# Kernel tuning notes

Hardware: AMD Instinct MI355X
Metric: run time of the kernel (lower is better)

## Reference

```python
import jax, jax.numpy as jnp
import numpy as np

NUM_EMBEDDINGS = 1024
EMBEDDING_DIM = 256
COMMITMENT_COST = 0.25
DECAY = 0.99
EPS = 1e-05
BATCH = 65536


def setup_inputs() -> dict:
    key = jax.random.key(0)
    k1, k2 = jax.random.split(key, 2)
    z_e = jax.random.normal(k1, (BATCH, EMBEDDING_DIM), dtype=jnp.float32)
    embedding = jax.random.normal(k2, (NUM_EMBEDDINGS, EMBEDDING_DIM), dtype=jnp.float32)
    ema_cluster_size = jnp.zeros((NUM_EMBEDDINGS,), dtype=jnp.float32)
    ema_w = embedding  # buffer initialized as a clone of the codebook
    return {"z_e": z_e, "embedding": embedding,
            "ema_cluster_size": ema_cluster_size, "ema_w": ema_w}


def reference(z_e, embedding, ema_cluster_size, ema_w):
    B, D = z_e.shape
    K = embedding.shape[0]

    # Squared L2 distances: ||z||^2 + ||e||^2 - 2 z.e  -> [B, K]
    z_sq = jnp.sum(z_e * z_e, axis=1, keepdims=True)          # [B, 1]
    e_sq = jnp.sum(embedding * embedding, axis=1)[None, :]    # [1, K]
    ze = jnp.matmul(z_e, embedding.T)                         # [B, K]
    distances = z_sq + e_sq - 2.0 * ze

    encoding_indices = jnp.argmin(distances, axis=1)          # [B]

    # Gather instead of one-hot matmul (same math as encodings @ embedding)
    z_q = embedding[encoding_indices]                         # [B, D]
    z_q_st = z_e + jax.lax.stop_gradient(z_q - z_e)

    vq_loss = COMMITMENT_COST * jnp.mean(
        (jax.lax.stop_gradient(z_q) - z_e) ** 2)

    # EMA statistics (training-mode update); segment_sum == one-hot reductions
    cluster_size = jax.ops.segment_sum(
        jnp.ones((B,), dtype=z_e.dtype), encoding_indices, num_segments=K)
    new_ema_cluster_size = DECAY * ema_cluster_size + (1.0 - DECAY) * cluster_size
    dw = jax.ops.segment_sum(z_e, encoding_indices, num_segments=K)  # [K, D]
    new_ema_w = DECAY * ema_w + (1.0 - DECAY) * dw

    n = jnp.sum(new_ema_cluster_size)
    smoothed = (new_ema_cluster_size + EPS) / (n + K * EPS) * n
    new_embedding = new_ema_w / smoothed[:, None]

    avg_probs = cluster_size / B
    perplexity = jnp.exp(-jnp.sum(avg_probs * jnp.log(avg_probs + 1e-10)))

    return (z_q_st, vq_loss, perplexity, encoding_indices,
            new_embedding, new_ema_cluster_size, new_ema_w)
```

## Files before the change

### kernel.cpp

```cpp
#include <hip/hip_runtime.h>
#include <hip/hip_bf16.h>
#include <math.h>

#define BATCH 65536
#define DIM 256
#define KC 1024
#define COMMIT 0.25f
#define DECAY 0.99f
#define EPSV 1e-5f

#define O_ZQ   0
#define O_LOSS 16777216
#define O_PERP 16777217
#define O_IDX  16777218
#define O_EMB  16842754
#define O_NCS  17104898
#define O_NEW  17105922

typedef __attribute__((ext_vector_type(8))) short bf16x8;
typedef __attribute__((ext_vector_type(4))) float f32x4;

typedef __attribute__((address_space(1))) const void* as1_cvp;
typedef __attribute__((address_space(3))) void* as3_vp;

__device__ __forceinline__ void gload_lds16(const void* g, void* l) {
    __builtin_amdgcn_global_load_lds((as1_cvp)g, (as3_vp)l, 16, 0, 0);
}

__device__ __forceinline__ unsigned short bf16_rne(float x) {
    unsigned u = __builtin_bit_cast(unsigned, x);
    unsigned r = (u + 0x7FFFu + ((u >> 16) & 1u)) >> 16;
    return (unsigned short)r;
}
__device__ __forceinline__ float bf16_to_f(unsigned short h) {
    unsigned u = ((unsigned)h) << 16;
    return __builtin_bit_cast(float, u);
}

__global__ __launch_bounds__(256) void zero_kernel(float* __restrict__ dw,
                                                   int* __restrict__ counts,
                                                   float* __restrict__ loss_part) {
    int i = blockIdx.x * 256 + threadIdx.x;
    if (i < KC * DIM) dw[i] = 0.0f;
    if (i < KC) counts[i] = 0;
    if (i < 256) loss_part[i] = 0.0f;
}

__global__ __launch_bounds__(64) void prep_kernel(const float* __restrict__ emb,
                                                  unsigned short* __restrict__ ehi,
                                                  unsigned short* __restrict__ elo,
                                                  float* __restrict__ e_sq) {
    int k = blockIdx.x;
    int lane = threadIdx.x;
    const float4* ep = (const float4*)(emb + (size_t)k * DIM);
    float4 e = ep[lane];
    float x[4] = {e.x, e.y, e.z, e.w};
    unsigned h[4], l[4];
    float s = 0.0f;
    #pragma unroll
    for (int j = 0; j < 4; ++j) {
        h[j] = bf16_rne(x[j]);
        l[j] = bf16_rne(x[j] - bf16_to_f((unsigned short)h[j]));
        s += x[j] * x[j];
    }
    uint2 ph = make_uint2(h[0] | (h[1] << 16), h[2] | (h[3] << 16));
    uint2 pl = make_uint2(l[0] | (l[1] << 16), l[2] | (l[3] << 16));
    int slot = lane >> 1;
    int half = lane & 1;
    int us = k * 256 + ((slot ^ (k & 7)) << 3) + (half << 2);
    *(uint2*)(ehi + us) = ph;
    *(uint2*)(elo + us) = pl;
    for (int off = 32; off; off >>= 1) s += __shfl_down(s, off, 64);
    if (lane == 0) e_sq[k] = s;
}

#define CH_ROWS 64
__global__ __launch_bounds__(256, 2) void argmin_kernel(
        const float* __restrict__ z_e,
        const unsigned short* __restrict__ ehi,
        const unsigned short* __restrict__ elo,
        const float* __restrict__ e_sq,
        int* __restrict__ idx_out, float* __restrict__ idx_f_out,
        int* __restrict__ counts) {
    __shared__ __align__(16) unsigned short bhi_s[CH_ROWS * 256];
    __shared__ __align__(16) unsigned short blo_s[CH_ROWS * 256];
    __shared__ float esq_s[KC];

    int tid = threadIdx.x;
    int w = tid >> 6;
    int lane = tid & 63;
    int m16 = lane & 15;
    int quad = lane >> 4;
    int base_m = blockIdx.x * 128 + w * 32;

    #pragma unroll
    for (int i = 0; i < 4; ++i) esq_s[tid + i * 256] = e_sq[tid + i * 256];

    bf16x8 ahi[2][8], alo[2][8];
    #pragma unroll
    for (int f = 0; f < 2; ++f) {
        const float* zr = z_e + (size_t)(base_m + f * 16 + m16) * DIM;
        #pragma unroll
        for (int ks = 0; ks < 8; ++ks) {
            const float4* p = (const float4*)(zr + ks * 32 + quad * 8);
            float4 x0 = p[0], x1 = p[1];
            float xs[8] = {x0.x, x0.y, x0.z, x0.w, x1.x, x1.y, x1.z, x1.w};
            #pragma unroll
            for (int j = 0; j < 8; ++j) {
                unsigned short h = bf16_rne(xs[j]);
                unsigned short l = bf16_rne(xs[j] - bf16_to_f(h));
                ahi[f][ks][j] = (short)h;
                alo[f][ks][j] = (short)l;
            }
        }
    }

    float best0[4] = {1e30f, 1e30f, 1e30f, 1e30f};
    float best1[4] = {1e30f, 1e30f, 1e30f, 1e30f};
    int bk0[4] = {0, 0, 0, 0};
    int bk1[4] = {0, 0, 0, 0};

    const int rsw = (m16 & 7) << 3;

    for (int chunk = 0; chunk < 16; ++chunk) {
        __syncthreads();
        {
            const char* gh = (const char*)ehi + chunk * 32768 + tid * 16;
            const char* gl = (const char*)elo + chunk * 32768 + tid * 16;
            char* lh = (char*)bhi_s + tid * 16;
            char* ll = (char*)blo_s + tid * 16;
            #pragma unroll
            for (int r = 0; r < 8; ++r) {
                gload_lds16(gh + r * 4096, lh + r * 4096);
                gload_lds16(gl + r * 4096, ll + r * 4096);
            }
        }
        __syncthreads();

        #pragma unroll
        for (int f = 0; f < 4; ++f) {
            f32x4 acc0 = {0.f, 0.f, 0.f, 0.f};
            f32x4 acc1 = {0.f, 0.f, 0.f, 0.f};
            const unsigned short* bh_row = bhi_s + (f * 16 + m16) * 256;
            const unsigned short* bl_row = blo_s + (f * 16 + m16) * 256;
            #pragma unroll
            for (int ks = 0; ks < 8; ++ks) {
                int us_off = (((ks * 4 + quad) << 3) ^ rsw);
                bf16x8 bh = *(const bf16x8*)(bh_row + us_off);
                bf16x8 bl = *(const bf16x8*)(bl_row + us_off);
                acc0 = __builtin_amdgcn_mfma_f32_16x16x32_bf16(ahi[0][ks], bh, acc0, 0, 0, 0);
                acc1 = __builtin_amdgcn_mfma_f32_16x16x32_bf16(ahi[1][ks], bh, acc1, 0, 0, 0);
                acc0 = __builtin_amdgcn_mfma_f32_16x16x32_bf16(ahi[0][ks], bl, acc0, 0, 0, 0);
                acc1 = __builtin_amdgcn_mfma_f32_16x16x32_bf16(ahi[1][ks], bl, acc1, 0, 0, 0);
                acc0 = __builtin_amdgcn_mfma_f32_16x16x32_bf16(alo[0][ks], bh, acc0, 0, 0, 0);
                acc1 = __builtin_amdgcn_mfma_f32_16x16x32_bf16(alo[1][ks], bh, acc1, 0, 0, 0);
            }
            int col = chunk * 64 + f * 16 + m16;
            float es = esq_s[col];
            #pragma unroll
            for (int r = 0; r < 4; ++r) {
                float d0 = es - 2.0f * acc0[r];
                float d1 = es - 2.0f * acc1[r];
                if (d0 < best0[r]) { best0[r] = d0; bk0[r] = col; }
                if (d1 < best1[r]) { best1[r] = d1; bk1[r] = col; }
            }
        }
    }

    #pragma unroll
    for (int off = 1; off < 16; off <<= 1) {
        #pragma unroll
        for (int r = 0; r < 4; ++r) {
            float ov0 = __shfl_xor(best0[r], off, 64);
            int   ok0 = __shfl_xor(bk0[r], off, 64);
            if (ov0 < best0[r] || (ov0 == best0[r] && ok0 < bk0[r])) { best0[r] = ov0; bk0[r] = ok0; }
            float ov1 = __shfl_xor(best1[r], off, 64);
            int   ok1 = __shfl_xor(bk1[r], off, 64);
            if (ov1 < best1[r] || (ov1 == best1[r] && ok1 < bk1[r])) { best1[r] = ov1; bk1[r] = ok1; }
        }
    }
    if (m16 == 0) {
        #pragma unroll
        for (int r = 0; r < 4; ++r) {
            int row0 = base_m + quad * 4 + r;
            int row1 = base_m + 16 + quad * 4 + r;
            idx_out[row0] = bk0[r];
            idx_f_out[row0] = (float)bk0[r];
            idx_out[row1] = bk1[r];
            idx_f_out[row1] = (float)bk1[r];
            atomicAdd(&counts[bk0[r]], 1);
            atomicAdd(&counts[bk1[r]], 1);
        }
    }
}

__global__ __launch_bounds__(1024) void prefix_kernel(const int* __restrict__ counts,
                                                      int* __restrict__ cursor) {
    __shared__ int sc[KC];
    int t = threadIdx.x;
    int c = counts[t];
    sc[t] = c;
    __syncthreads();
    for (int off = 1; off < KC; off <<= 1) {
        int v = 0;
        if (t >= off) v = sc[t - off];
        __syncthreads();
        if (t >= off) sc[t] += v;
        __syncthreads();
    }
    cursor[t] = sc[t] - c;
}

__global__ __launch_bounds__(256) void scatter_rows_kernel(
        const int* __restrict__ idx, int* __restrict__ cursor,
        int* __restrict__ sorted_rows) {
    int i = blockIdx.x * 256 + threadIdx.x;
    int k = idx[i];
    int pos = atomicAdd(&cursor[k], 1);
    sorted_rows[pos] = i;
}

#define SEG 64
__global__ __launch_bounds__(256) void dw_zq_kernel(
        const float* __restrict__ z_e, const float* __restrict__ emb,
        const int* __restrict__ idx, const int* __restrict__ sorted_rows,
        float* __restrict__ zq_out, float* __restrict__ dw,
        float* __restrict__ loss_part) {
    __shared__ int rows_s[SEG];
    __shared__ int keys_s[SEG];
    int t = threadIdx.x;
    int base = blockIdx.x * SEG;
    if (t < SEG) {
        int r = sorted_rows[base + t];
        rows_s[t] = r;
        keys_s[t] = idx[r];
    }
    __syncthreads();

    float acc = 0.0f;
    float lsum = 0.0f;
    int kprev = keys_s[0];
    for (int g = 0; g < SEG / 8; ++g) {
        int rowb[8], kb[8];
        float zb[8], qb[8];
        #pragma unroll
        for (int u = 0; u < 8; ++u) {
            int i = g * 8 + u;
            rowb[u] = rows_s[i];
            kb[u] = keys_s[i];
        }
        #pragma unroll
        for (int u = 0; u < 8; ++u) {
            zb[u] = z_e[(size_t)rowb[u] * DIM + t];
            qb[u] = emb[(size_t)kb[u] * DIM + t];
        }
        #pragma unroll
        for (int u = 0; u < 8; ++u) {
            float z = zb[u];
            float d = qb[u] - z;
            zq_out[(size_t)rowb[u] * DIM + t] = z + d;
            lsum += d * d;
            int k = kb[u];
            if (k != kprev) {
                atomicAdd(&dw[(size_t)kprev * DIM + t], acc);
                acc = 0.0f;
                kprev = k;
            }
            acc += z;
        }
    }
    atomicAdd(&dw[(size_t)kprev * DIM + t], acc);

    __shared__ float red[256];
    red[t] = lsum;
    __syncthreads();
    for (int s = 128; s; s >>= 1) {
        if (t < s) red[t] += red[t + s];
        __syncthreads();
    }
    if (t == 0) atomicAdd(&loss_part[blockIdx.x & 255], red[0]);
}

__global__ __launch_bounds__(1024) void finalize_cluster(
        const float* __restrict__ ema_cs, const int* __restrict__ counts,
        const float* __restrict__ loss_part, float* __restrict__ out,
        float* __restrict__ n_ws) {
    __shared__ float s1[1024];
    __shared__ float s2[1024];
    __shared__ float s3[1024];
    int t = threadIdx.x;
    float c = (float)counts[t];
    float ncs = DECAY * ema_cs[t] + (1.0f - DECAY) * c;
    out[O_NCS + t] = ncs;
    float p = c / (float)BATCH;
    s1[t] = ncs;
    s2[t] = p * logf(p + 1e-10f);
    s3[t] = (t < 256) ? loss_part[t] : 0.0f;
    __syncthreads();
    for (int s = 512; s; s >>= 1) {
        if (t < s) { s1[t] += s1[t + s]; s2[t] += s2[t + s]; s3[t] += s3[t + s]; }
        __syncthreads();
    }
    if (t == 0) {
        n_ws[0] = s1[0];
        out[O_PERP] = expf(-s2[0]);
        out[O_LOSS] = COMMIT * s3[0] / (float)((size_t)BATCH * DIM);
    }
}

__global__ __launch_bounds__(256) void finalize_emb(
        const float* __restrict__ ema_w, const float* __restrict__ dw,
        const float* __restrict__ ncs_arr, const float* __restrict__ n_ws,
        float* __restrict__ out_emb, float* __restrict__ out_emaw) {
    int k = blockIdx.x;
    int d = threadIdx.x;
    size_t i = (size_t)k * DIM + d;
    float w = DECAY * ema_w[i] + (1.0f - DECAY) * dw[i];
    out_emaw[i] = w;
    float n = n_ws[0];
    float ncs = ncs_arr[k];
    float smoothed = (ncs + EPSV) / (n + (float)KC * EPSV) * n;
    out_emb[i] = w / smoothed;
}

extern "C" void kernel_launch(void* const* d_in, const int* in_sizes, int n_in,
                              void* d_out, int out_size, void* d_ws, size_t ws_size,
                              hipStream_t stream) {
    const float* z_e    = (const float*)d_in[0];
    const float* emb    = (const float*)d_in[1];
    const float* ema_cs = (const float*)d_in[2];
    const float* ema_w  = (const float*)d_in[3];
    float* out = (float*)d_out;
    float* ws = (float*)d_ws;

    float* dw            = ws;
    unsigned short* ehi  = (unsigned short*)(dw + KC * DIM);
    unsigned short* elo  = ehi + KC * DIM;
    float* e_sq          = (float*)(elo + KC * DIM);
    int* idx             = (int*)(e_sq + KC);
    int* counts          = idx + BATCH;
    int* cursor          = counts + KC;
    int* sorted_rows     = cursor + KC;
    float* loss_part     = (float*)(sorted_rows + BATCH);
    float* n_ws          = loss_part + 256;

    zero_kernel<<<dim3(1024), dim3(256), 0, stream>>>(dw, counts, loss_part);
    prep_kernel<<<dim3(KC), dim3(64), 0, stream>>>(emb, ehi, elo, e_sq);
    argmin_kernel<<<dim3(BATCH / 128), dim3(256), 0, stream>>>(
        z_e, ehi, elo, e_sq, idx, out + O_IDX, counts);
    prefix_kernel<<<dim3(1), dim3(1024), 0, stream>>>(counts, cursor);
    scatter_rows_kernel<<<dim3(BATCH / 256), dim3(256), 0, stream>>>(
        idx, cursor, sorted_rows);
    dw_zq_kernel<<<dim3(BATCH / SEG), dim3(256), 0, stream>>>(
        z_e, emb, idx, sorted_rows, out + O_ZQ, dw, loss_part);
    finalize_cluster<<<dim3(1), dim3(1024), 0, stream>>>(
        ema_cs, counts, loss_part, out, n_ws);
    finalize_emb<<<dim3(KC), dim3(256), 0, stream>>>(
        ema_w, dw, out + O_NCS, n_ws, out + O_EMB, out + O_NEW);
}
```

Before: 300.1 us.

## Double-buffer codebook chunks in argmin, fuse prep/zero, vectorize dw and scan

The argmin kernel now splits the codebook into 32-row chunks held in two LDS buffers, so the next chunk's global-to-LDS load is issued while the current chunk runs on MFMA. The zero and prep kernels are merged into one launch. The prefix scan uses wave shuffles instead of a barrier-heavy shared-memory loop. The gather/scatter kernel has each wave handle 16 sorted rows with float4 loads, which cuts per-thread load count but issues four scalar atomics per flush.

```diff
diff --git a/kernel.cpp b/kernel.cpp
--- a/kernel.cpp
+++ b/kernel.cpp
@@ -37,44 +37,42 @@
     return __builtin_bit_cast(float, u);
 }
 
-__global__ __launch_bounds__(256) void zero_kernel(float* __restrict__ dw,
-                                                   int* __restrict__ counts,
-                                                   float* __restrict__ loss_part) {
-    int i = blockIdx.x * 256 + threadIdx.x;
-    if (i < KC * DIM) dw[i] = 0.0f;
-    if (i < KC) counts[i] = 0;
-    if (i < 256) loss_part[i] = 0.0f;
-}
-
-__global__ __launch_bounds__(64) void prep_kernel(const float* __restrict__ emb,
-                                                  unsigned short* __restrict__ ehi,
-                                                  unsigned short* __restrict__ elo,
-                                                  float* __restrict__ e_sq) {
+__global__ __launch_bounds__(256) void prep_zero_kernel(
+        const float* __restrict__ emb,
+        unsigned short* __restrict__ ehi, unsigned short* __restrict__ elo,
+        float* __restrict__ e_sq, float* __restrict__ dw,
+        int* __restrict__ counts, float* __restrict__ loss_part) {
     int k = blockIdx.x;
-    int lane = threadIdx.x;
-    const float4* ep = (const float4*)(emb + (size_t)k * DIM);
-    float4 e = ep[lane];
-    float x[4] = {e.x, e.y, e.z, e.w};
-    unsigned h[4], l[4];
-    float s = 0.0f;
-    #pragma unroll
-    for (int j = 0; j < 4; ++j) {
-        h[j] = bf16_rne(x[j]);
-        l[j] = bf16_rne(x[j] - bf16_to_f((unsigned short)h[j]));
-        s += x[j] * x[j];
-    }
-    uint2 ph = make_uint2(h[0] | (h[1] << 16), h[2] | (h[3] << 16));
-    uint2 pl = make_uint2(l[0] | (l[1] << 16), l[2] | (l[3] << 16));
-    int slot = lane >> 1;
-    int half = lane & 1;
-    int us = k * 256 + ((slot ^ (k & 7)) << 3) + (half << 2);
-    *(uint2*)(ehi + us) = ph;
-    *(uint2*)(elo + us) = pl;
-    for (int off = 32; off; off >>= 1) s += __shfl_down(s, off, 64);
-    if (lane == 0) e_sq[k] = s;
-}
-
-#define CH_ROWS 64
+    int t = threadIdx.x;
+    dw[(size_t)k * DIM + t] = 0.0f;
+    if (t == 64) counts[k] = 0;
+    if (k < 2 && t >= 128) loss_part[k * 128 + (t - 128)] = 0.0f;
+    if (t < 64) {
+        int lane = t;
+        const float4* ep = (const float4*)(emb + (size_t)k * DIM);
+        float4 e = ep[lane];
+        float x[4] = {e.x, e.y, e.z, e.w};
+        unsigned h[4], l[4];
+        float s = 0.0f;
+        #pragma unroll
+        for (int j = 0; j < 4; ++j) {
+            h[j] = bf16_rne(x[j]);
+            l[j] = bf16_rne(x[j] - bf16_to_f((unsigned short)h[j]));
+            s += x[j] * x[j];
+        }
+        uint2 ph = make_uint2(h[0] | (h[1] << 16), h[2] | (h[3] << 16));
+        uint2 pl = make_uint2(l[0] | (l[1] << 16), l[2] | (l[3] << 16));
+        int slot = lane >> 1;
+        int half = lane & 1;
+        int us = k * 256 + ((slot ^ (k & 7)) << 3) + (half << 2);
+        *(uint2*)(ehi + us) = ph;
+        *(uint2*)(elo + us) = pl;
+        for (int off = 32; off; off >>= 1) s += __shfl_down(s, off, 64);
+        if (lane == 0) e_sq[k] = s;
+    }
+}
+
+#define CH_ROWS 32
 __global__ __launch_bounds__(256, 2) void argmin_kernel(
         const float* __restrict__ z_e,
         const unsigned short* __restrict__ ehi,
@@ -82,8 +80,8 @@
         const float* __restrict__ e_sq,
         int* __restrict__ idx_out, float* __restrict__ idx_f_out,
         int* __restrict__ counts) {
-    __shared__ __align__(16) unsigned short bhi_s[CH_ROWS * 256];
-    __shared__ __align__(16) unsigned short blo_s[CH_ROWS * 256];
+    __shared__ __align__(16) unsigned short bhi_s[2][CH_ROWS * 256];
+    __shared__ __align__(16) unsigned short blo_s[2][CH_ROWS * 256];
     __shared__ float esq_s[KC];
 
     int tid = threadIdx.x;
@@ -92,6 +90,17 @@
     int m16 = lane & 15;
     int quad = lane >> 4;
     int base_m = blockIdx.x * 128 + w * 32;
+
+#define STAGE(c, b) { \
+    const char* gh_ = (const char*)ehi + (c) * 16384 + tid * 16; \
+    const char* gl_ = (const char*)elo + (c) * 16384 + tid * 16; \
+    char* lh_ = (char*)(bhi_s[b]) + tid * 16; \
+    char* ll_ = (char*)(blo_s[b]) + tid * 16; \
+    _Pragma("unroll") for (int r_ = 0; r_ < 4; ++r_) { \
+        gload_lds16(gh_ + r_ * 4096, lh_ + r_ * 4096); \
+        gload_lds16(gl_ + r_ * 4096, ll_ + r_ * 4096); } }
+
+    STAGE(0, 0)
 
     #pragma unroll
     for (int i = 0; i < 4; ++i) esq_s[tid + i * 256] = e_sq[tid + i * 256];
@@ -122,49 +131,39 @@
 
     const int rsw = (m16 & 7) << 3;
 
-    for (int chunk = 0; chunk < 16; ++chunk) {
+#define COMPUTE(c, b) { \
+    _Pragma("unroll") for (int f_ = 0; f_ < 2; ++f_) { \
+        f32x4 acc0 = {0.f, 0.f, 0.f, 0.f}; \
+        f32x4 acc1 = {0.f, 0.f, 0.f, 0.f}; \
+        const unsigned short* bh_row = bhi_s[b] + (f_ * 16 + m16) * 256; \
+        const unsigned short* bl_row = blo_s[b] + (f_ * 16 + m16) * 256; \
+        _Pragma("unroll") for (int ks_ = 0; ks_ < 8; ++ks_) { \
+            int us_off = (((ks_ * 4 + quad) << 3) ^ rsw); \
+            bf16x8 bh = *(const bf16x8*)(bh_row + us_off); \
+            bf16x8 bl = *(const bf16x8*)(bl_row + us_off); \
+            acc0 = __builtin_amdgcn_mfma_f32_16x16x32_bf16(ahi[0][ks_], bh, acc0, 0, 0, 0); \
+            acc1 = __builtin_amdgcn_mfma_f32_16x16x32_bf16(ahi[1][ks_], bh, acc1, 0, 0, 0); \
+            acc0 = __builtin_amdgcn_mfma_f32_16x16x32_bf16(ahi[0][ks_], bl, acc0, 0, 0, 0); \
+            acc1 = __builtin_amdgcn_mfma_f32_16x16x32_bf16(ahi[1][ks_], bl, acc1, 0, 0, 0); \
+            acc0 = __builtin_amdgcn_mfma_f32_16x16x32_bf16(alo[0][ks_], bh, acc0, 0, 0, 0); \
+            acc1 = __builtin_amdgcn_mfma_f32_16x16x32_bf16(alo[1][ks_], bh, acc1, 0, 0, 0); } \
+        int col = (c) * 32 + f_ * 16 + m16; \
+        float es = esq_s[col]; \
+        _Pragma("unroll") for (int r_ = 0; r_ < 4; ++r_) { \
+            float d0 = es - 2.0f * acc0[r_]; \
+            float d1 = es - 2.0f * acc1[r_]; \
+            if (d0 < best0[r_]) { best0[r_] = d0; bk0[r_] = col; } \
+            if (d1 < best1[r_]) { best1[r_] = d1; bk1[r_] = col; } } } }
+
+    __syncthreads();
+
+    for (int c = 0; c < 32; c += 2) {
+        STAGE(c + 1, 1)
+        COMPUTE(c, 0)
         __syncthreads();
-        {
-            const char* gh = (const char*)ehi + chunk * 32768 + tid * 16;
-            const char* gl = (const char*)elo + chunk * 32768 + tid * 16;
-            char* lh = (char*)bhi_s + tid * 16;
-            char* ll = (char*)blo_s + tid * 16;
-            #pragma unroll
-            for (int r = 0; r < 8; ++r) {
-                gload_lds16(gh + r * 4096, lh + r * 4096);
-                gload_lds16(gl + r * 4096, ll + r * 4096);
-            }
-        }
+        if (c + 2 < 32) STAGE(c + 2, 0)
+        COMPUTE(c + 1, 1)
         __syncthreads();
-
-        #pragma unroll
-        for (int f = 0; f < 4; ++f) {
-            f32x4 acc0 = {0.f, 0.f, 0.f, 0.f};
-            f32x4 acc1 = {0.f, 0.f, 0.f, 0.f};
-            const unsigned short* bh_row = bhi_s + (f * 16 + m16) * 256;
-            const unsigned short* bl_row = blo_s + (f * 16 + m16) * 256;
-            #pragma unroll
-            for (int ks = 0; ks < 8; ++ks) {
-                int us_off = (((ks * 4 + quad) << 3) ^ rsw);
-                bf16x8 bh = *(const bf16x8*)(bh_row + us_off);
-                bf16x8 bl = *(const bf16x8*)(bl_row + us_off);
-                acc0 = __builtin_amdgcn_mfma_f32_16x16x32_bf16(ahi[0][ks], bh, acc0, 0, 0, 0);
-                acc1 = __builtin_amdgcn_mfma_f32_16x16x32_bf16(ahi[1][ks], bh, acc1, 0, 0, 0);
-                acc0 = __builtin_amdgcn_mfma_f32_16x16x32_bf16(ahi[0][ks], bl, acc0, 0, 0, 0);
-                acc1 = __builtin_amdgcn_mfma_f32_16x16x32_bf16(ahi[1][ks], bl, acc1, 0, 0, 0);
-                acc0 = __builtin_amdgcn_mfma_f32_16x16x32_bf16(alo[0][ks], bh, acc0, 0, 0, 0);
-                acc1 = __builtin_amdgcn_mfma_f32_16x16x32_bf16(alo[1][ks], bh, acc1, 0, 0, 0);
-            }
-            int col = chunk * 64 + f * 16 + m16;
-            float es = esq_s[col];
-            #pragma unroll
-            for (int r = 0; r < 4; ++r) {
-                float d0 = es - 2.0f * acc0[r];
-                float d1 = es - 2.0f * acc1[r];
-                if (d0 < best0[r]) { best0[r] = d0; bk0[r] = col; }
-                if (d1 < best1[r]) { best1[r] = d1; bk1[r] = col; }
-            }
-        }
     }
 
     #pragma unroll
@@ -192,23 +191,37 @@
             atomicAdd(&counts[bk1[r]], 1);
         }
     }
+#undef STAGE
+#undef COMPUTE
 }
 
 __global__ __launch_bounds__(1024) void prefix_kernel(const int* __restrict__ counts,
                                                       int* __restrict__ cursor) {
-    __shared__ int sc[KC];
+    __shared__ int wsum[16];
     int t = threadIdx.x;
+    int lane = t & 63;
+    int wv = t >> 6;
     int c = counts[t];
-    sc[t] = c;
-    __syncthreads();
-    for (int off = 1; off < KC; off <<= 1) {
-        int v = 0;
-        if (t >= off) v = sc[t - off];
-        __syncthreads();
-        if (t >= off) sc[t] += v;
-        __syncthreads();
-    }
-    cursor[t] = sc[t] - c;
+    int x = c;
+    #pragma unroll
+    for (int off = 1; off < 64; off <<= 1) {
+        int v = __shfl_up(x, off, 64);
+        if (lane >= off) x += v;
+    }
+    if (lane == 63) wsum[wv] = x;
+    __syncthreads();
+    if (wv == 0) {
+        int v = (lane < 16) ? wsum[lane] : 0;
+        #pragma unroll
+        for (int off = 1; off < 16; off <<= 1) {
+            int u = __shfl_up(v, off, 64);
+            if (lane >= off) v += u;
+        }
+        if (lane < 16) wsum[lane] = v;
+    }
+    __syncthreads();
+    int woff = (wv == 0) ? 0 : wsum[wv - 1];
+    cursor[t] = woff + x - c;
 }
 
 __global__ __launch_bounds__(256) void scatter_rows_kernel(
@@ -229,6 +242,8 @@
     __shared__ int rows_s[SEG];
     __shared__ int keys_s[SEG];
     int t = threadIdx.x;
+    int w = t >> 6;
+    int lane = t & 63;
     int base = blockIdx.x * SEG;
     if (t < SEG) {
         int r = sorted_rows[base + t];
@@ -237,39 +252,51 @@
     }
     __syncthreads();
 
-    float acc = 0.0f;
+    int c4 = lane * 4;
+    float4 acc = make_float4(0.f, 0.f, 0.f, 0.f);
     float lsum = 0.0f;
-    int kprev = keys_s[0];
-    for (int g = 0; g < SEG / 8; ++g) {
+    int kprev = keys_s[w * 16];
+    #pragma unroll
+    for (int g = 0; g < 2; ++g) {
         int rowb[8], kb[8];
-        float zb[8], qb[8];
+        float4 zb[8], qb[8];
         #pragma unroll
         for (int u = 0; u < 8; ++u) {
-            int i = g * 8 + u;
+            int i = w * 16 + g * 8 + u;
             rowb[u] = rows_s[i];
             kb[u] = keys_s[i];
         }
         #pragma unroll
         for (int u = 0; u < 8; ++u) {
-            zb[u] = z_e[(size_t)rowb[u] * DIM + t];
-            qb[u] = emb[(size_t)kb[u] * DIM + t];
+            zb[u] = *(const float4*)(z_e + (size_t)rowb[u] * DIM + c4);
+            qb[u] = *(const float4*)(emb + (size_t)kb[u] * DIM + c4);
         }
         #pragma unroll
         for (int u = 0; u < 8; ++u) {
-            float z = zb[u];
-            float d = qb[u] - z;
-            zq_out[(size_t)rowb[u] * DIM + t] = z + d;
-            lsum += d * d;
-            int k = kb[u];
-            if (k != kprev) {
-                atomicAdd(&dw[(size_t)kprev * DIM + t], acc);
-                acc = 0.0f;
-                kprev = k;
+            float4 z = zb[u], q = qb[u];
+            float4 d = make_float4(q.x - z.x, q.y - z.y, q.z - z.z, q.w - z.w);
+            float4 o = make_float4(z.x + d.x, z.y + d.y, z.z + d.z, z.w + d.w);
+            *(float4*)(zq_out + (size_t)rowb[u] * DIM + c4) = o;
+            lsum += d.x * d.x + d.y * d.y + d.z * d.z + d.w * d.w;
+            if (kb[u] != kprev) {
+                float* dst = dw + (size_t)kprev * DIM + c4;
+                atomicAdd(dst + 0, acc.x);
+                atomicAdd(dst + 1, acc.y);
+                atomicAdd(dst + 2, acc.z);
+                atomicAdd(dst + 3, acc.w);
+                acc = make_float4(0.f, 0.f, 0.f, 0.f);
+                kprev = kb[u];
             }
-            acc += z;
-        }
-    }
-    atomicAdd(&dw[(size_t)kprev * DIM + t], acc);
+            acc.x += z.x; acc.y += z.y; acc.z += z.z; acc.w += z.w;
+        }
+    }
+    {
+        float* dst = dw + (size_t)kprev * DIM + c4;
+        atomicAdd(dst + 0, acc.x);
+        atomicAdd(dst + 1, acc.y);
+        atomicAdd(dst + 2, acc.z);
+        atomicAdd(dst + 3, acc.w);
+    }
 
     __shared__ float red[256];
     red[t] = lsum;
@@ -344,8 +371,8 @@
     float* loss_part     = (float*)(sorted_rows + BATCH);
     float* n_ws          = loss_part + 256;
 
-    zero_kernel<<<dim3(1024), dim3(256), 0, stream>>>(dw, counts, loss_part);
-    prep_kernel<<<dim3(KC), dim3(64), 0, stream>>>(emb, ehi, elo, e_sq);
+    prep_zero_kernel<<<dim3(KC), dim3(256), 0, stream>>>(
+        emb, ehi, elo, e_sq, dw, counts, loss_part);
     argmin_kernel<<<dim3(BATCH / 128), dim3(256), 0, stream>>>(
         z_e, ehi, elo, e_sq, idx, out + O_IDX, counts);
     prefix_kernel<<<dim3(1), dim3(1024), 0, stream>>>(counts, cursor);
```

Measured after the change: 318.9 us. 6.3% more time.
